# Kernel optimization log

Measured on AMD Instinct MI355X. Metric: run time of the kernel, lower is better.

Reference implementation:

```python
import math
import jax, jax.numpy as jnp
import numpy as np

N_ORDERS = 2
CHUNK = 64  # tokens per chunk (before virtual-token expansion)


def _expand_derivative(x, n):
    """expand_virtual_tokens(mode='derivative'): [B,H,S,D] -> [B,H,S*n,D]."""
    B, H, S, D = x.shape
    pad = jnp.zeros((B, H, n - 1, D), x.dtype)
    xp = jnp.concatenate([pad, x], axis=2)  # [B,H,S+n-1,D]
    coeffs = np.array([(-1) ** kk * math.comb(n - 1, kk) for kk in range(n)], dtype=np.float32)
    coeffs = coeffs / np.abs(coeffs).sum()  # L1-normalized binomial coeffs
    # window j at token t is x_pad[t+j]*coeffs[j]; then flip window dim (as in torch .flip(-1))
    win = jnp.stack([xp[:, :, j:j + S, :] * coeffs[j] for j in range(n)], axis=3)  # [B,H,S,n,D]
    win = win[:, :, :, ::-1, :]
    return win.reshape(B, H, S * n, D)


def _unlinear(x, scale=2.0):
    """unlinear_activation: gated norm-scaled gelu applied to inter-chunk state."""
    xn = jnp.linalg.norm(x, axis=-1, keepdims=True) + 1e-6
    return x / scale * jax.nn.gelu(scale * x / xn, approximate=True)


def _stab(x):
    # ensure_stability: clamp to [-1e4, 1e4], nan -> center (0)
    return jnp.nan_to_num(jnp.clip(x, -1e4, 1e4), nan=0.0, posinf=1e4, neginf=-1e4)


def _forward(q, k, v, beta):
    n = N_ORDERS
    B, H, S, D = q.shape
    qe = _expand_derivative(q, n)
    ke = _expand_derivative(k, n)
    ve = _expand_derivative(v, n)
    be = jnp.repeat(beta, n, axis=-1)[..., None]  # [B,H,S*n,1]
    w = ke * be  # delta-rule write keys
    u = ve * be  # delta-rule write values

    Cn = CHUNK * n                     # virtual tokens per chunk
    NC = (S * n) // Cn                 # number of chunks
    ch = lambda x: x.reshape(B, H, NC, Cn, D)
    qc, kc, wc, uc = ch(qe), ch(ke), ch(w), ch(u)

    # triangular (forward-substitution) inversion per chunk:
    # T = (I + tril(W K^T, -1))^{-1}  == fast_invert_matrix of the strictly-lower system
    A = jnp.tril(jnp.einsum('bhnid,bhnjd->bhnij', wc, kc), -1)
    eye = jnp.eye(Cn, dtype=q.dtype)
    T = jax.scipy.linalg.solve_triangular(
        eye + A, jnp.broadcast_to(eye, A.shape), lower=True, unit_diagonal=True)
    wci = jnp.einsum('bhnij,bhnjd->bhnid', T, wc)
    uci = jnp.einsum('bhnij,bhnjd->bhnid', T, uc)

    def chunk_step(h, xs):
        # sequential_delta_product_scan body: per-token Householder updates, n_orders steps
        qx, wx, ux = xs  # each [B,H,Cn,D]
        C = CHUNK
        qr = qx.reshape(B, H, C, n, D)
        wr = wx.reshape(B, H, C, n, D)
        ur = ux.reshape(B, H, C, n, D)
        state = jnp.broadcast_to(h[:, :, None], (B, H, C, D, D))  # per-token state
        outs = []
        for s in range(n):
            qs, ws, us = qr[:, :, :, s], wr[:, :, :, s], ur[:, :, :, s]
            kho = jnp.einsum('bhcd,bhcde->bhce', ws, state)
            uval = us - kho
            o_inter = jnp.einsum('bhcd,bhcde->bhce', qs, state)
            o_intra = qs * uval
            state = _stab(state + jnp.einsum('bhcd,bhce->bhcde', ws, uval))
            outs.append(o_intra + o_inter)
        o = jnp.stack(outs, axis=3).reshape(B, H, C * n, D)  # interleave: pos t*n+s
        h_new = _unlinear(state[:, :, -1])  # linear_activation=False path
        return h_new, o

    xs = (jnp.moveaxis(qc, 2, 0), jnp.moveaxis(wci, 2, 0), jnp.moveaxis(uci, 2, 0))
    h0 = jnp.zeros((B, H, D, D), q.dtype)
    _, os = jax.lax.scan(chunk_step, h0, xs)  # os: [NC,B,H,Cn,D]
    out_v = jnp.moveaxis(os, 0, 2).reshape(B, H, S, n, D)
    return out_v[..., n - 1, :]  # collapse virtual tokens: keep last-order output per token


def setup_inputs() -> dict:
    key = jax.random.key(0)
    kq, kk, kv, kb = jax.random.split(key, 4)
    B, H, S, D = 2, 16, 2048, 64
    return {
        'q': jax.random.normal(kq, (B, H, S, D), jnp.float32),
        'k': jax.random.normal(kk, (B, H, S, D), jnp.float32),
        'v': jax.random.normal(kv, (B, H, S, D), jnp.float32),
        'beta': jax.random.uniform(kb, (B, H, S), jnp.float32),
    }


def reference(q, k, v, beta):
    return _forward(q, k, v, beta)
```

## Files before the change

kernel.cpp:

```cpp
#include <hip/hip_runtime.h>
#include <math.h>


namespace {
constexpr int PAIRS = 32;
constexpr int SLEN  = 2048;
constexpr int D     = 64;
constexpr int CK    = 64;
constexpr int CN    = 128;
constexpr int NCH   = 32;
constexpr int NB2   = 16;
constexpr int NP    = 5;

__device__ __forceinline__ float stab1(float x) {
    float y = __builtin_amdgcn_fmed3f(x, -10000.f, 10000.f);
    return (x != x) ? 0.f : y;
}

__device__ __forceinline__ int kidx(int a, int f4) {
    return a * 68 + 4 * (f4 ^ ((a >> 2) & 3));
}
}

__global__ __launch_bounds__(512, 1)
void la_phase1(const float* __restrict__ kg, const float* __restrict__ vg,
               const float* __restrict__ bg, float* __restrict__ ws)
{
    __shared__ float Ysh[CN][CN];
    __shared__ float Gm[65][66];
    __shared__ char  ureg[36864];
    __shared__ float bq4[CK], bh[CK];

    float* kstf = (float*)ureg;
    float* scm  = (float*)ureg;
    float (*redsh)[3][8][CN] = (float(*)[3][8][CN])(ureg + 12288);

    const int blk  = blockIdx.x;
    const int p    = blk >> 5;
    const int nc   = blk & 31;
    const int tid  = threadIdx.x;
    const int baseT = nc * CK;
    const float* kp = kg + (size_t)p * SLEN * D;
    const float* vp = vg + (size_t)p * SLEN * D;
    const float* bp = bg + (size_t)p * SLEN;

    for (int u = tid; u < 65 * 16; u += 512) {
        int a = u >> 4, f4 = u & 15;
        int src = baseT - 1 + a;
        float4 val = float4{0.f, 0.f, 0.f, 0.f};
        if (src >= 0) val = ((const float4*)(kp + (size_t)src * D))[f4];
        *(float4*)&kstf[kidx(a, f4)] = val;
    }
    if (tid < CK) {
        float bv = bp[baseT + tid];
        bq4[tid] = 0.25f * bv;
        bh[tid]  = 0.5f  * bv;
    }
    __syncthreads();

    for (int u = tid; u < CN * 32; u += 512) {
        int i = u >> 5, f4i = u & 31;
        int ci = i >> 1, si = i & 1;
        float sc = si ? bh[ci] : -bh[ci];
        float4 val = float4{0.f, 0.f, 0.f, 0.f};
        if (f4i < 16) {
            val = *(const float4*)&kstf[kidx(ci - si + 1, f4i)];
        } else {
            int srcT = baseT + ci - si;
            if (srcT >= 0) val = ((const float4*)(vp + (size_t)srcT * D))[f4i - 16];
        }
        val.x *= sc; val.y *= sc; val.z *= sc; val.w *= sc;
        *(float4*)&Ysh[i][f4i * 4] = val;
    }

    for (int tt = tid; tt < 17 * 17; tt += 512) {
        int ta = tt / 17, tb = tt % 17;
        if (tb > ta) continue;
        int a0 = ta * 4, b0 = tb * 4;
        float acc[4][4] = {};
        for (int d4 = 0; d4 < 16; ++d4) {
            float4 av[4], bv[4];
            #pragma unroll
            for (int r = 0; r < 4; ++r) {
                av[r] = *(const float4*)&kstf[kidx(min(a0 + r, 64), d4)];
                bv[r] = *(const float4*)&kstf[kidx(min(b0 + r, 64), d4)];
            }
            #pragma unroll
            for (int r = 0; r < 4; ++r)
                #pragma unroll
                for (int c = 0; c < 4; ++c)
                    acc[r][c] += av[r].x * bv[c].x + av[r].y * bv[c].y
                               + av[r].z * bv[c].z + av[r].w * bv[c].w;
        }
        #pragma unroll
        for (int r = 0; r < 4; ++r)
            #pragma unroll
            for (int c = 0; c < 4; ++c)
                if (a0 + r <= 64 && b0 + c <= 64) {
                    Gm[a0 + r][b0 + c] = acc[r][c];
                    Gm[b0 + c][a0 + r] = acc[r][c];
                }
    }
    __syncthreads();

    for (int e = tid; e < 192; e += 512) {
        int gp = (e < 64) ? 0 : 1;
        int ee = e - gp * 64;
        int j = ee >> 3, r = ee & 7;
        int i = 8 * gp + r;
        int ai = (i >> 1) - (i & 1) + 1;
        int aj = (j >> 1) - (j & 1) + 1;
        float sgn = ((i ^ j) & 1) ? -1.f : 1.f;
        scm[(gp * CN + j) * 8 + r] = sgn * bq4[i >> 1] * Gm[ai][aj];
    }
    __syncthreads();

    const int col = tid & 127;
    const int grp = tid >> 7;

    for (int g = 0; g < 16; ++g) {
        const int bufG  = g % 3;
        const int bufG1 = (g + 1) % 3;
        const int bufG2 = (g + 2) % 3;

        if (grp == 0) {
            float acc[8] = {};
            if (g > 0) {
                #pragma unroll
                for (int r = 0; r < 8; ++r)
                    acc[r] = redsh[g & 1][0][r][col] + redsh[g & 1][1][r][col]
                           + redsh[g & 1][2][r][col];
                #pragma unroll
                for (int jj = 0; jj < 8; ++jj) {
                    int j = 8 * g - 8 + jj;
                    float yv = Ysh[j][col];
                    const float4 a03 = *(const float4*)&scm[(bufG * CN + j) * 8];
                    const float4 a47 = *(const float4*)&scm[(bufG * CN + j) * 8 + 4];
                    acc[0] += a03.x * yv; acc[1] += a03.y * yv;
                    acc[2] += a03.z * yv; acc[3] += a03.w * yv;
                    acc[4] += a47.x * yv; acc[5] += a47.y * yv;
                    acc[6] += a47.z * yv; acc[7] += a47.w * yv;
                }
            }
            float yn[8];
            #pragma unroll
            for (int r = 0; r < 8; ++r) {
                float val = Ysh[8 * g + r][col] - acc[r];
                #pragma unroll
                for (int rp = 0; rp < 8; ++rp)
                    if (rp < r) val -= scm[(bufG * CN + 8 * g + rp) * 8 + r] * yn[rp];
                yn[r] = val;
                Ysh[8 * g + r][col] = val;
            }
        } else {
            if (g + 2 <= 15) {
                int gb = g + 2, jmax = 8 * gb + 8;
                for (int e = tid - 128; e < 8 * jmax; e += 384) {
                    int j = e >> 3, r = e & 7;
                    int i = 8 * gb + r;
                    int ai = (i >> 1) - (i & 1) + 1;
                    int aj = (j >> 1) - (j & 1) + 1;
                    float sgn = ((i ^ j) & 1) ? -1.f : 1.f;
                    scm[(bufG2 * CN + j) * 8 + r] = sgn * bq4[i >> 1] * Gm[ai][aj];
                }
            }
            if (g + 1 <= 15) {
                float acc[8] = {};
                for (int j = grp - 1; j < 8 * g; j += 3) {
                    float yv = Ysh[j][col];
                    const float4 a03 = *(const float4*)&scm[(bufG1 * CN + j) * 8];
                    const float4 a47 = *(const float4*)&scm[(bufG1 * CN + j) * 8 + 4];
                    acc[0] += a03.x * yv; acc[1] += a03.y * yv;
                    acc[2] += a03.z * yv; acc[3] += a03.w * yv;
                    acc[4] += a47.x * yv; acc[5] += a47.y * yv;
                    acc[6] += a47.z * yv; acc[7] += a47.w * yv;
                }
                #pragma unroll
                for (int r = 0; r < 8; ++r)
                    redsh[(g + 1) & 1][grp - 1][r][col] = acc[r];
            }
        }
        __syncthreads();
    }

    float* gY = ws + (size_t)(p * NCH + nc) * (CN * CN);
    for (int u = tid; u < CN * 32; u += 512) {
        int r = u >> 5, f4 = u & 31;
        *(float4*)&gY[r * CN + f4 * 4] = *(const float4*)&Ysh[r][f4 * 4];
    }
}

__global__ __launch_bounds__(512, 4)
void la_phase2(const float* __restrict__ qg, const float* __restrict__ ws,
               float* __restrict__ outg)
{
    __shared__ float WU[2][NP][256];
    __shared__ float Qs[2][NP][64];
    __shared__ float pR1[8][NP][64];
    __shared__ float pKH[8][NP][64];
    __shared__ float pOA[8][NP][64];
    __shared__ float UV0[NP][64];
    __shared__ float UV1r[64];
    __shared__ float hsh[64][67];

    const int blk  = blockIdx.x;
    const int p    = blk >> 4, nb = blk & 15;
    const int tid  = threadIdx.x;
    const int w    = tid >> 6, lane = tid & 63;
    const int hd   = tid >> 3;
    const int he0  = (tid & 7) * 8;

    const float* qp = qg + (size_t)p * SLEN * D;
    float* op = outg + (size_t)p * SLEN * D;
    const float* wsbase = ws + (size_t)p * NCH * (CN * CN);

    const int cMain = nb * 4 + w;

    float4 wuR = float4{0.f, 0.f, 0.f, 0.f};
    float  qR  = 0.f;

    auto stage_load = [&](int nc) {
        const float* gY = wsbase + (size_t)nc * (CN * CN);
        if (w < 4) {
            wuR = *(const float4*)(gY + (size_t)(2 * cMain) * CN + lane * 4);
            int t = nc * CK + cMain;
            qR = qp[(size_t)((t > 0) ? t - 1 : 0) * D + lane];
        } else if (w == 4) {
            wuR = *(const float4*)(gY + (size_t)126 * CN + lane * 4);
            qR = qp[(size_t)(nc * CK + 62) * D + lane];
        }
    };
    auto stage_write = [&](int buf) {
        if (w < NP) {
            *(float4*)&WU[buf][w][lane * 4] = wuR;
            Qs[buf][w][lane] = qR;
        }
    };

    for (int idx = tid; idx < 64 * 67; idx += 512) (&hsh[0][0])[idx] = 0.f;
    stage_load(0);
    stage_write(0);
    __syncthreads();

    for (int nc = 0; nc < NCH; ++nc) {
        const int buf = nc & 1;

        float hs[8];
        #pragma unroll
        for (int j = 0; j < 8; ++j) hs[j] = hsh[8 * w + j][lane];

        if (nc + 1 < NCH) stage_load(nc + 1);

        #pragma unroll
        for (int P = 0; P < NP; ++P) {
            float4 a = *(const float4*)&WU[buf][P][8 * w];
            float4 b = *(const float4*)&WU[buf][P][8 * w + 4];
            pR1[w][P][lane] =
                  ((a.x * hs[0] + a.y * hs[1]) + (a.z * hs[2] + a.w * hs[3]))
                + ((b.x * hs[4] + b.y * hs[5]) + (b.z * hs[6] + b.w * hs[7]));
        }
        __syncthreads();

        if (w < NP) {
            float s = 0.f;
            #pragma unroll
            for (int wv = 0; wv < 8; ++wv) s += pR1[wv][w][lane];
            UV0[w][lane] = WU[buf][w][64 + lane] - s;
        }
        __syncthreads();

        #pragma unroll
        for (int P = 0; P < NP; ++P) {
            float uv0 = UV0[P][lane];
            float4 w0a = *(const float4*)&WU[buf][P][8 * w];
            float4 w0b = *(const float4*)&WU[buf][P][8 * w + 4];
            float4 w1a = *(const float4*)&WU[buf][P][128 + 8 * w];
            float4 w1b = *(const float4*)&WU[buf][P][128 + 8 * w + 4];
            float4 qa  = *(const float4*)&Qs[buf][P][8 * w];
            float4 qb  = *(const float4*)&Qs[buf][P][8 * w + 4];
            float st0 = stab1(hs[0] + w0a.x * uv0);
            float st1 = stab1(hs[1] + w0a.y * uv0);
            float st2 = stab1(hs[2] + w0a.z * uv0);
            float st3 = stab1(hs[3] + w0a.w * uv0);
            float st4 = stab1(hs[4] + w0b.x * uv0);
            float st5 = stab1(hs[5] + w0b.y * uv0);
            float st6 = stab1(hs[6] + w0b.z * uv0);
            float st7 = stab1(hs[7] + w0b.w * uv0);
            pKH[w][P][lane] =
                  ((w1a.x * st0 + w1a.y * st1) + (w1a.z * st2 + w1a.w * st3))
                + ((w1b.x * st4 + w1b.y * st5) + (w1b.z * st6 + w1b.w * st7));
            pOA[w][P][lane] =
                  ((qa.x * st0 + qa.y * st1) + (qa.z * st2 + qa.w * st3))
                + ((qb.x * st4 + qb.y * st5) + (qb.z * st6 + qb.w * st7));
        }
        stage_write(buf ^ 1);
        __syncthreads();

        if (w < 4) {
            float skh = 0.f, soa = 0.f;
            #pragma unroll
            for (int wv = 0; wv < 8; ++wv) {
                skh += pKH[wv][w][lane];
                soa += pOA[wv][w][lane];
            }
            float uv1 = WU[buf][w][192 + lane] - skh;
            int t = nc * CK + cMain;
            float outv = 0.5f * (Qs[buf][w][lane] * uv1 + soa);
            op[(size_t)t * D + lane] = (t > 0) ? outv : 0.f;
        } else if (w == 4) {
            float skh = 0.f;
            #pragma unroll
            for (int wv = 0; wv < 8; ++wv) skh += pKH[wv][4][lane];
            UV1r[lane] = WU[buf][4][192 + lane] - skh;
        }
        __syncthreads();

        {
            float w0d = WU[buf][4][hd];
            float w1d = WU[buf][4][128 + hd];
            float st2v[8];
            float ssum = 0.f;
            #pragma unroll
            for (int j = 0; j < 8; ++j) {
                float st1 = stab1(hsh[hd][he0 + j] + w0d * UV0[4][he0 + j]);
                float st2 = stab1(st1 + w1d * UV1r[he0 + j]);
                st2v[j] = st2;
                ssum += st2 * st2;
            }
            ssum += __shfl_xor(ssum, 1);
            ssum += __shfl_xor(ssum, 2);
            ssum += __shfl_xor(ssum, 4);
            float xn = __builtin_amdgcn_sqrtf(ssum) + 1e-6f;
            float s2 = 2.f * __builtin_amdgcn_rcpf(xn);
            #pragma unroll
            for (int j = 0; j < 8; ++j) {
                float x  = st2v[j];
                float y  = x * s2;
                float y2 = y * y;
                float e  = __builtin_amdgcn_exp2f(y * (2.3022078f + 0.1029432f * y2));
                float th = (e - 1.f) * __builtin_amdgcn_rcpf(e + 1.f);
                hsh[hd][he0 + j] = 0.25f * x * y * (1.f + th);
            }
        }
        __syncthreads();
    }
}

extern "C" void kernel_launch(void* const* d_in, const int* in_sizes, int n_in,
                              void* d_out, int out_size, void* d_ws, size_t ws_size,
                              hipStream_t stream)
{
    (void)in_sizes; (void)n_in; (void)out_size; (void)ws_size;
    const float* q    = (const float*)d_in[0];
    const float* k    = (const float*)d_in[1];
    const float* v    = (const float*)d_in[2];
    const float* beta = (const float*)d_in[3];
    float* ws  = (float*)d_ws;
    float* out = (float*)d_out;

    la_phase1<<<PAIRS * NCH, 512, 0, stream>>>(k, v, beta, ws);
    la_phase2<<<PAIRS * NB2, 512, 0, stream>>>(q, ws, out);
}
```

Baseline: 275.1 us.

## Split phase-1 triangular solve across two blocks by column half

Result: no change. 280.5 us (+2.0%).

```diff
diff --git a/kernel.cpp b/kernel.cpp
--- a/kernel.cpp
+++ b/kernel.cpp
@@ -22,29 +22,30 @@
 }
 }
 
-__global__ __launch_bounds__(512, 1)
+__global__ __launch_bounds__(256, 2)
 void la_phase1(const float* __restrict__ kg, const float* __restrict__ vg,
                const float* __restrict__ bg, float* __restrict__ ws)
 {
-    __shared__ float Ysh[CN][CN];
+    __shared__ float Ysh[CN][68];
     __shared__ float Gm[65][66];
-    __shared__ char  ureg[36864];
+    __shared__ char  ureg[24576];
     __shared__ float bq4[CK], bh[CK];
 
     float* kstf = (float*)ureg;
     float* scm  = (float*)ureg;
-    float (*redsh)[3][8][CN] = (float(*)[3][8][CN])(ureg + 12288);
+    float (*redsh)[3][8][64] = (float(*)[3][8][64])(ureg + 12288);
 
     const int blk  = blockIdx.x;
-    const int p    = blk >> 5;
-    const int nc   = blk & 31;
+    const int p    = blk >> 6;
+    const int nc   = (blk >> 1) & 31;
+    const int half = blk & 1;
     const int tid  = threadIdx.x;
     const int baseT = nc * CK;
     const float* kp = kg + (size_t)p * SLEN * D;
     const float* vp = vg + (size_t)p * SLEN * D;
     const float* bp = bg + (size_t)p * SLEN;
 
-    for (int u = tid; u < 65 * 16; u += 512) {
+    for (int u = tid; u < 65 * 16; u += 256) {
         int a = u >> 4, f4 = u & 15;
         int src = baseT - 1 + a;
         float4 val = float4{0.f, 0.f, 0.f, 0.f};
@@ -58,22 +59,22 @@
     }
     __syncthreads();
 
-    for (int u = tid; u < CN * 32; u += 512) {
-        int i = u >> 5, f4i = u & 31;
+    for (int u = tid; u < CN * 16; u += 256) {
+        int i = u >> 4, f4 = u & 15;
         int ci = i >> 1, si = i & 1;
         float sc = si ? bh[ci] : -bh[ci];
         float4 val = float4{0.f, 0.f, 0.f, 0.f};
-        if (f4i < 16) {
-            val = *(const float4*)&kstf[kidx(ci - si + 1, f4i)];
+        if (half == 0) {
+            val = *(const float4*)&kstf[kidx(ci - si + 1, f4)];
         } else {
             int srcT = baseT + ci - si;
-            if (srcT >= 0) val = ((const float4*)(vp + (size_t)srcT * D))[f4i - 16];
+            if (srcT >= 0) val = ((const float4*)(vp + (size_t)srcT * D))[f4];
         }
         val.x *= sc; val.y *= sc; val.z *= sc; val.w *= sc;
-        *(float4*)&Ysh[i][f4i * 4] = val;
-    }
-
-    for (int tt = tid; tt < 17 * 17; tt += 512) {
+        *(float4*)&Ysh[i][f4 * 4] = val;
+    }
+
+    for (int tt = tid; tt < 17 * 17; tt += 256) {
         int ta = tt / 17, tb = tt % 17;
         if (tb > ta) continue;
         int a0 = ta * 4, b0 = tb * 4;
@@ -103,7 +104,7 @@
     }
     __syncthreads();
 
-    for (int e = tid; e < 192; e += 512) {
+    for (int e = tid; e < 192; e += 256) {
         int gp = (e < 64) ? 0 : 1;
         int ee = e - gp * 64;
         int j = ee >> 3, r = ee & 7;
@@ -115,15 +116,15 @@
     }
     __syncthreads();
 
-    const int col = tid & 127;
-    const int grp = tid >> 7;
+    const int col = tid & 63;
+    const int m   = tid >> 6;
 
     for (int g = 0; g < 16; ++g) {
         const int bufG  = g % 3;
         const int bufG1 = (g + 1) % 3;
         const int bufG2 = (g + 2) % 3;
 
-        if (grp == 0) {
+        if (m == 0) {
             float acc[8] = {};
             if (g > 0) {
                 #pragma unroll
@@ -155,7 +156,7 @@
         } else {
             if (g + 2 <= 15) {
                 int gb = g + 2, jmax = 8 * gb + 8;
-                for (int e = tid - 128; e < 8 * jmax; e += 384) {
+                for (int e = tid - 64; e < 8 * jmax; e += 192) {
                     int j = e >> 3, r = e & 7;
                     int i = 8 * gb + r;
                     int ai = (i >> 1) - (i & 1) + 1;
@@ -166,7 +167,32 @@
             }
             if (g + 1 <= 15) {
                 float acc[8] = {};
-                for (int j = grp - 1; j < 8 * g; j += 3) {
+                const int len = (8 * g + 2) / 3;
+                const int lo = (m - 1) * len;
+                const int hi = min(8 * g, lo + len);
+                int j = lo;
+                for (; j + 4 <= hi; j += 4) {
+                    float y0 = Ysh[j][col], y1 = Ysh[j + 1][col];
+                    float y2 = Ysh[j + 2][col], y3 = Ysh[j + 3][col];
+                    const float* s0 = &scm[(bufG1 * CN + j) * 8];
+                    const float4 a0 = *(const float4*)(s0);
+                    const float4 b0 = *(const float4*)(s0 + 4);
+                    const float4 a1 = *(const float4*)(s0 + 8);
+                    const float4 b1 = *(const float4*)(s0 + 12);
+                    const float4 a2 = *(const float4*)(s0 + 16);
+                    const float4 b2 = *(const float4*)(s0 + 20);
+                    const float4 a3 = *(const float4*)(s0 + 24);
+                    const float4 b3 = *(const float4*)(s0 + 28);
+                    acc[0] += a0.x * y0 + a1.x * y1 + a2.x * y2 + a3.x * y3;
+                    acc[1] += a0.y * y0 + a1.y * y1 + a2.y * y2 + a3.y * y3;
+                    acc[2] += a0.z * y0 + a1.z * y1 + a2.z * y2 + a3.z * y3;
+                    acc[3] += a0.w * y0 + a1.w * y1 + a2.w * y2 + a3.w * y3;
+                    acc[4] += b0.x * y0 + b1.x * y1 + b2.x * y2 + b3.x * y3;
+                    acc[5] += b0.y * y0 + b1.y * y1 + b2.y * y2 + b3.y * y3;
+                    acc[6] += b0.z * y0 + b1.z * y1 + b2.z * y2 + b3.z * y3;
+                    acc[7] += b0.w * y0 + b1.w * y1 + b2.w * y2 + b3.w * y3;
+                }
+                for (; j < hi; ++j) {
                     float yv = Ysh[j][col];
                     const float4 a03 = *(const float4*)&scm[(bufG1 * CN + j) * 8];
                     const float4 a47 = *(const float4*)&scm[(bufG1 * CN + j) * 8 + 4];
@@ -177,15 +203,15 @@
                 }
                 #pragma unroll
                 for (int r = 0; r < 8; ++r)
-                    redsh[(g + 1) & 1][grp - 1][r][col] = acc[r];
-            }
-        }
-        __syncthreads();
-    }
-
-    float* gY = ws + (size_t)(p * NCH + nc) * (CN * CN);
-    for (int u = tid; u < CN * 32; u += 512) {
-        int r = u >> 5, f4 = u & 31;
+                    redsh[(g + 1) & 1][m - 1][r][col] = acc[r];
+            }
+        }
+        __syncthreads();
+    }
+
+    float* gY = ws + (size_t)(p * NCH + nc) * (CN * CN) + half * 64;
+    for (int u = tid; u < CN * 16; u += 256) {
+        int r = u >> 4, f4 = u & 15;
         *(float4*)&gY[r * CN + f4 * 4] = *(const float4*)&Ysh[r][f4 * 4];
     }
 }
@@ -358,6 +384,6 @@
     float* ws  = (float*)d_ws;
     float* out = (float*)d_out;
 
-    la_phase1<<<PAIRS * NCH, 512, 0, stream>>>(k, v, beta, ws);
+    la_phase1<<<PAIRS * NCH * 2, 256, 0, stream>>>(k, v, beta, ws);
     la_phase2<<<PAIRS * NB2, 512, 0, stream>>>(q, ws, out);
 }
```

## Keep phase-1 triangular-solve rows in registers and shrink block to 256 threads

Applied to the files above, without the earlier changes.

New measurement: 439.2 us. 1.6x slower.

```diff
diff --git a/kernel.cpp b/kernel.cpp
--- a/kernel.cpp
+++ b/kernel.cpp
@@ -20,31 +20,54 @@
 __device__ __forceinline__ int kidx(int a, int f4) {
     return a * 68 + 4 * (f4 ^ ((a >> 2) & 3));
 }
-}
-
-__global__ __launch_bounds__(512, 1)
+
+template<int GI>
+__device__ __forceinline__ void solve_group(float (&y0)[32], float (&y1)[32],
+                                            float (&accA)[8], float (&accB)[8],
+                                            const float* scmDiag) {
+    float yn0[8], yn1[8];
+    #pragma unroll
+    for (int r = 0; r < 8; ++r) {
+        float v0 = y0[GI * 8 + r] - accA[r];
+        float v1 = y1[GI * 8 + r] - accB[r];
+        #pragma unroll
+        for (int rp = 0; rp < 8; ++rp) {
+            if (rp < r) {
+                float a = scmDiag[rp * 8 + r];
+                v0 -= a * yn0[rp];
+                v1 -= a * yn1[rp];
+            }
+        }
+        yn0[r] = v0; yn1[r] = v1;
+        y0[GI * 8 + r] = v0; y1[GI * 8 + r] = v1;
+    }
+}
+}
+
+__global__ __launch_bounds__(256, 3)
 void la_phase1(const float* __restrict__ kg, const float* __restrict__ vg,
                const float* __restrict__ bg, float* __restrict__ ws)
 {
-    __shared__ float Ysh[CN][CN];
     __shared__ float Gm[65][66];
-    __shared__ char  ureg[36864];
+    __shared__ char  uni[28672];
     __shared__ float bq4[CK], bh[CK];
 
-    float* kstf = (float*)ureg;
-    float* scm  = (float*)ureg;
-    float (*redsh)[3][8][CN] = (float(*)[3][8][CN])(ureg + 12288);
+    float* kstf = (float*)uni;
+    float* scm  = (float*)uni;
+    float (*redsh)[8][CN] = (float(*)[8][CN])(uni + 12288);
 
     const int blk  = blockIdx.x;
     const int p    = blk >> 5;
     const int nc   = blk & 31;
     const int tid  = threadIdx.x;
+    const int lane = tid & 63;
+    const int m    = tid >> 6;
     const int baseT = nc * CK;
     const float* kp = kg + (size_t)p * SLEN * D;
     const float* vp = vg + (size_t)p * SLEN * D;
     const float* bp = bg + (size_t)p * SLEN;
 
-    for (int u = tid; u < 65 * 16; u += 512) {
+    for (int u = tid; u < 65 * 16; u += 256) {
         int a = u >> 4, f4 = u & 15;
         int src = baseT - 1 + a;
         float4 val = float4{0.f, 0.f, 0.f, 0.f};
@@ -58,22 +81,7 @@
     }
     __syncthreads();
 
-    for (int u = tid; u < CN * 32; u += 512) {
-        int i = u >> 5, f4i = u & 31;
-        int ci = i >> 1, si = i & 1;
-        float sc = si ? bh[ci] : -bh[ci];
-        float4 val = float4{0.f, 0.f, 0.f, 0.f};
-        if (f4i < 16) {
-            val = *(const float4*)&kstf[kidx(ci - si + 1, f4i)];
-        } else {
-            int srcT = baseT + ci - si;
-            if (srcT >= 0) val = ((const float4*)(vp + (size_t)srcT * D))[f4i - 16];
-        }
-        val.x *= sc; val.y *= sc; val.z *= sc; val.w *= sc;
-        *(float4*)&Ysh[i][f4i * 4] = val;
-    }
-
-    for (int tt = tid; tt < 17 * 17; tt += 512) {
+    for (int tt = tid; tt < 17 * 17; tt += 256) {
         int ta = tt / 17, tb = tt % 17;
         if (tb > ta) continue;
         int a0 = ta * 4, b0 = tb * 4;
@@ -101,9 +109,34 @@
                     Gm[b0 + c][a0 + r] = acc[r][c];
                 }
     }
+
+    float y0[32], y1[32];
+    #pragma unroll
+    for (int gi = 0; gi < 4; ++gi) {
+        #pragma unroll
+        for (int r8 = 0; r8 < 8; ++r8) {
+            int i = 8 * (4 * gi + m) + r8;
+            int ci = i >> 1, si = i & 1;
+            float sc = si ? bh[ci] : -bh[ci];
+            float2 val;
+            if (lane < 32) {
+                int a = ci - si + 1;
+                int e = 2 * lane;
+                int idx = a * 68 + 4 * ((e >> 2) ^ ((a >> 2) & 3)) + (e & 3);
+                val = *(const float2*)&kstf[idx];
+            } else {
+                int srcT = baseT + ci - si;
+                int e = 2 * (lane - 32);
+                if (srcT >= 0) val = *(const float2*)&vp[(size_t)srcT * D + e];
+                else           val = float2{0.f, 0.f};
+            }
+            y0[gi * 8 + r8] = sc * val.x;
+            y1[gi * 8 + r8] = sc * val.y;
+        }
+    }
     __syncthreads();
 
-    for (int e = tid; e < 192; e += 512) {
+    for (int e = tid; e < 192; e += 256) {
         int gp = (e < 64) ? 0 : 1;
         int ee = e - gp * 64;
         int j = ee >> 3, r = ee & 7;
@@ -115,79 +148,80 @@
     }
     __syncthreads();
 
-    const int col = tid & 127;
-    const int grp = tid >> 7;
-
     for (int g = 0; g < 16; ++g) {
-        const int bufG  = g % 3;
-        const int bufG1 = (g + 1) % 3;
-        const int bufG2 = (g + 2) % 3;
-
-        if (grp == 0) {
-            float acc[8] = {};
+        const int s = g & 3;
+        if (m == s) {
+            float accA[8] = {}, accB[8] = {};
             if (g > 0) {
                 #pragma unroll
-                for (int r = 0; r < 8; ++r)
-                    acc[r] = redsh[g & 1][0][r][col] + redsh[g & 1][1][r][col]
-                           + redsh[g & 1][2][r][col];
-                #pragma unroll
-                for (int jj = 0; jj < 8; ++jj) {
-                    int j = 8 * g - 8 + jj;
-                    float yv = Ysh[j][col];
-                    const float4 a03 = *(const float4*)&scm[(bufG * CN + j) * 8];
-                    const float4 a47 = *(const float4*)&scm[(bufG * CN + j) * 8 + 4];
-                    acc[0] += a03.x * yv; acc[1] += a03.y * yv;
-                    acc[2] += a03.z * yv; acc[3] += a03.w * yv;
-                    acc[4] += a47.x * yv; acc[5] += a47.y * yv;
-                    acc[6] += a47.z * yv; acc[7] += a47.w * yv;
+                for (int wv = 0; wv < 4; ++wv)
+                    #pragma unroll
+                    for (int r = 0; r < 8; ++r) {
+                        float2 t = *(const float2*)&redsh[wv][r][2 * lane];
+                        accA[r] += t.x; accB[r] += t.y;
+                    }
+            }
+            const float* scmDiag = scm + (((g % 3) * CN + 8 * g) * 8);
+            const int gq = g >> 2;
+            if      (gq == 0) solve_group<0>(y0, y1, accA, accB, scmDiag);
+            else if (gq == 1) solve_group<1>(y0, y1, accA, accB, scmDiag);
+            else if (gq == 2) solve_group<2>(y0, y1, accA, accB, scmDiag);
+            else              solve_group<3>(y0, y1, accA, accB, scmDiag);
+        } else if (g + 2 <= 15) {
+            const int T2 = g + 2, bufB = T2 % 3;
+            const int br = (m < s ? m : m - 1) * 64 + lane;
+            const int nel = 8 * (8 * T2 + 8);
+            for (int e = br; e < nel; e += 192) {
+                int j = e >> 3, r = e & 7;
+                int i = 8 * T2 + r;
+                int ai = (i >> 1) - (i & 1) + 1;
+                int aj = (j >> 1) - (j & 1) + 1;
+                float sgn = ((i ^ j) & 1) ? -1.f : 1.f;
+                scm[(bufB * CN + j) * 8 + r] = sgn * bq4[i >> 1] * Gm[ai][aj];
+            }
+        }
+        __syncthreads();
+
+        if (g < 15) {
+            const int bufT = (g + 1) % 3;
+            float accA[8] = {}, accB[8] = {};
+            #pragma unroll
+            for (int gi = 0; gi < 4; ++gi) {
+                if (4 * gi + m <= g) {
+                    #pragma unroll
+                    for (int r8 = 0; r8 < 8; ++r8) {
+                        int j = 8 * (4 * gi + m) + r8;
+                        const float* sp = &scm[(bufT * CN + j) * 8];
+                        const float4 a03 = *(const float4*)(sp);
+                        const float4 a47 = *(const float4*)(sp + 4);
+                        float yv0 = y0[gi * 8 + r8], yv1 = y1[gi * 8 + r8];
+                        accA[0] += a03.x * yv0; accB[0] += a03.x * yv1;
+                        accA[1] += a03.y * yv0; accB[1] += a03.y * yv1;
+                        accA[2] += a03.z * yv0; accB[2] += a03.z * yv1;
+                        accA[3] += a03.w * yv0; accB[3] += a03.w * yv1;
+                        accA[4] += a47.x * yv0; accB[4] += a47.x * yv1;
+                        accA[5] += a47.y * yv0; accB[5] += a47.y * yv1;
+                        accA[6] += a47.z * yv0; accB[6] += a47.z * yv1;
+                        accA[7] += a47.w * yv0; accB[7] += a47.w * yv1;
+                    }
                 }
             }
-            float yn[8];
-            #pragma unroll
-            for (int r = 0; r < 8; ++r) {
-                float val = Ysh[8 * g + r][col] - acc[r];
-                #pragma unroll
-                for (int rp = 0; rp < 8; ++rp)
-                    if (rp < r) val -= scm[(bufG * CN + 8 * g + rp) * 8 + r] * yn[rp];
-                yn[r] = val;
-                Ysh[8 * g + r][col] = val;
-            }
-        } else {
-            if (g + 2 <= 15) {
-                int gb = g + 2, jmax = 8 * gb + 8;
-                for (int e = tid - 128; e < 8 * jmax; e += 384) {
-                    int j = e >> 3, r = e & 7;
-                    int i = 8 * gb + r;
-                    int ai = (i >> 1) - (i & 1) + 1;
-                    int aj = (j >> 1) - (j & 1) + 1;
-                    float sgn = ((i ^ j) & 1) ? -1.f : 1.f;
-                    scm[(bufG2 * CN + j) * 8 + r] = sgn * bq4[i >> 1] * Gm[ai][aj];
-                }
-            }
-            if (g + 1 <= 15) {
-                float acc[8] = {};
-                for (int j = grp - 1; j < 8 * g; j += 3) {
-                    float yv = Ysh[j][col];
-                    const float4 a03 = *(const float4*)&scm[(bufG1 * CN + j) * 8];
-                    const float4 a47 = *(const float4*)&scm[(bufG1 * CN + j) * 8 + 4];
-                    acc[0] += a03.x * yv; acc[1] += a03.y * yv;
-                    acc[2] += a03.z * yv; acc[3] += a03.w * yv;
-                    acc[4] += a47.x * yv; acc[5] += a47.y * yv;
-                    acc[6] += a47.z * yv; acc[7] += a47.w * yv;
-                }
-                #pragma unroll
-                for (int r = 0; r < 8; ++r)
-                    redsh[(g + 1) & 1][grp - 1][r][col] = acc[r];
-            }
+            #pragma unroll
+            for (int r = 0; r < 8; ++r)
+                *(float2*)&redsh[m][r][2 * lane] = float2{accA[r], accB[r]};
         }
         __syncthreads();
     }
 
     float* gY = ws + (size_t)(p * NCH + nc) * (CN * CN);
-    for (int u = tid; u < CN * 32; u += 512) {
-        int r = u >> 5, f4 = u & 31;
-        *(float4*)&gY[r * CN + f4 * 4] = *(const float4*)&Ysh[r][f4 * 4];
-    }
+    #pragma unroll
+    for (int gi = 0; gi < 4; ++gi)
+        #pragma unroll
+        for (int r8 = 0; r8 < 8; ++r8) {
+            int j = 8 * (4 * gi + m) + r8;
+            *(float2*)&gY[(size_t)j * CN + 2 * lane] =
+                float2{y0[gi * 8 + r8], y1[gi * 8 + r8]};
+        }
 }
 
 __global__ __launch_bounds__(512, 4)
@@ -358,6 +392,6 @@
     float* ws  = (float*)d_ws;
     float* out = (float*)d_out;
 
-    la_phase1<<<PAIRS * NCH, 512, 0, stream>>>(k, v, beta, ws);
+    la_phase1<<<PAIRS * NCH, 256, 0, stream>>>(k, v, beta, ws);
     la_phase2<<<PAIRS * NB2, 512, 0, stream>>>(q, ws, out);
 }
```

## Split phase-1 triangular solve across two blocks per chunk by column half

Applied to the files above, without the earlier changes.

New measurement: 347.3 us. +26.3%, slower.

```diff
diff --git a/kernel.cpp b/kernel.cpp
--- a/kernel.cpp
+++ b/kernel.cpp
@@ -22,23 +22,26 @@
 }
 }
 
-__global__ __launch_bounds__(512, 1)
+__global__ __launch_bounds__(512, 2)
 void la_phase1(const float* __restrict__ kg, const float* __restrict__ vg,
                const float* __restrict__ bg, float* __restrict__ ws)
 {
-    __shared__ float Ysh[CN][CN];
-    __shared__ float Gm[65][66];
-    __shared__ char  ureg[36864];
+    __shared__ float Ysh[CN][65];
+    __shared__ float Gm[65][72];
+    __shared__ char  uni[26624];
     __shared__ float bq4[CK], bh[CK];
 
-    float* kstf = (float*)ureg;
-    float* scm  = (float*)ureg;
-    float (*redsh)[3][8][CN] = (float(*)[3][8][CN])(ureg + 12288);
+    float* kstf = (float*)uni;
+    float* scm  = (float*)uni;
+    float (*redsh)[64][9] = (float(*)[64][9])(uni + 8192);
 
     const int blk  = blockIdx.x;
-    const int p    = blk >> 5;
-    const int nc   = blk & 31;
+    const int p    = blk >> 6;
+    const int nc   = (blk >> 1) & 31;
+    const int half = blk & 1;
     const int tid  = threadIdx.x;
+    const int lane = tid & 63;
+    const int m    = tid >> 6;
     const int baseT = nc * CK;
     const float* kp = kg + (size_t)p * SLEN * D;
     const float* vp = vg + (size_t)p * SLEN * D;
@@ -58,19 +61,19 @@
     }
     __syncthreads();
 
-    for (int u = tid; u < CN * 32; u += 512) {
-        int i = u >> 5, f4i = u & 31;
+    for (int u = tid; u < CN * 16; u += 512) {
+        int i = u >> 4, f4 = u & 15;
         int ci = i >> 1, si = i & 1;
         float sc = si ? bh[ci] : -bh[ci];
         float4 val = float4{0.f, 0.f, 0.f, 0.f};
-        if (f4i < 16) {
-            val = *(const float4*)&kstf[kidx(ci - si + 1, f4i)];
+        if (half == 0) {
+            val = *(const float4*)&kstf[kidx(ci - si + 1, f4)];
         } else {
             int srcT = baseT + ci - si;
-            if (srcT >= 0) val = ((const float4*)(vp + (size_t)srcT * D))[f4i - 16];
+            if (srcT >= 0) val = ((const float4*)(vp + (size_t)srcT * D))[f4];
         }
         val.x *= sc; val.y *= sc; val.z *= sc; val.w *= sc;
-        *(float4*)&Ysh[i][f4i * 4] = val;
+        *(float4*)&Ysh[i][f4 * 4] = val;
     }
 
     for (int tt = tid; tt < 17 * 17; tt += 512) {
@@ -103,89 +106,80 @@
     }
     __syncthreads();
 
-    for (int e = tid; e < 192; e += 512) {
-        int gp = (e < 64) ? 0 : 1;
-        int ee = e - gp * 64;
-        int j = ee >> 3, r = ee & 7;
-        int i = 8 * gp + r;
+    for (int e = tid; e < 64; e += 512) {
+        int j = e >> 3, r = e & 7;
+        int i = r;
         int ai = (i >> 1) - (i & 1) + 1;
         int aj = (j >> 1) - (j & 1) + 1;
         float sgn = ((i ^ j) & 1) ? -1.f : 1.f;
-        scm[(gp * CN + j) * 8 + r] = sgn * bq4[i >> 1] * Gm[ai][aj];
+        scm[j * 8 + r] = sgn * bq4[i >> 1] * Gm[ai][aj];
     }
     __syncthreads();
 
-    const int col = tid & 127;
-    const int grp = tid >> 7;
-
     for (int g = 0; g < 16; ++g) {
-        const int bufG  = g % 3;
-        const int bufG1 = (g + 1) % 3;
-        const int bufG2 = (g + 2) % 3;
-
-        if (grp == 0) {
+        const int s = g & 7;
+        if (m == s) {
             float acc[8] = {};
             if (g > 0) {
                 #pragma unroll
-                for (int r = 0; r < 8; ++r)
-                    acc[r] = redsh[g & 1][0][r][col] + redsh[g & 1][1][r][col]
-                           + redsh[g & 1][2][r][col];
-                #pragma unroll
-                for (int jj = 0; jj < 8; ++jj) {
-                    int j = 8 * g - 8 + jj;
-                    float yv = Ysh[j][col];
-                    const float4 a03 = *(const float4*)&scm[(bufG * CN + j) * 8];
-                    const float4 a47 = *(const float4*)&scm[(bufG * CN + j) * 8 + 4];
-                    acc[0] += a03.x * yv; acc[1] += a03.y * yv;
-                    acc[2] += a03.z * yv; acc[3] += a03.w * yv;
-                    acc[4] += a47.x * yv; acc[5] += a47.y * yv;
-                    acc[6] += a47.z * yv; acc[7] += a47.w * yv;
+                for (int wv = 0; wv < 8; ++wv) {
+                    float4 t0 = *(const float4*)&redsh[wv][lane][0];
+                    float4 t1 = *(const float4*)&redsh[wv][lane][4];
+                    acc[0] += t0.x; acc[1] += t0.y; acc[2] += t0.z; acc[3] += t0.w;
+                    acc[4] += t1.x; acc[5] += t1.y; acc[6] += t1.z; acc[7] += t1.w;
                 }
             }
+            const float* sd = &scm[(((g & 1) * CN) + 8 * g) * 8];
             float yn[8];
             #pragma unroll
             for (int r = 0; r < 8; ++r) {
-                float val = Ysh[8 * g + r][col] - acc[r];
+                float val = Ysh[8 * g + r][lane] - acc[r];
                 #pragma unroll
                 for (int rp = 0; rp < 8; ++rp)
-                    if (rp < r) val -= scm[(bufG * CN + 8 * g + rp) * 8 + r] * yn[rp];
+                    if (rp < r) val -= sd[rp * 8 + r] * yn[rp];
                 yn[r] = val;
-                Ysh[8 * g + r][col] = val;
-            }
-        } else {
-            if (g + 2 <= 15) {
-                int gb = g + 2, jmax = 8 * gb + 8;
-                for (int e = tid - 128; e < 8 * jmax; e += 384) {
-                    int j = e >> 3, r = e & 7;
-                    int i = 8 * gb + r;
-                    int ai = (i >> 1) - (i & 1) + 1;
-                    int aj = (j >> 1) - (j & 1) + 1;
-                    float sgn = ((i ^ j) & 1) ? -1.f : 1.f;
-                    scm[(bufG2 * CN + j) * 8 + r] = sgn * bq4[i >> 1] * Gm[ai][aj];
-                }
-            }
-            if (g + 1 <= 15) {
-                float acc[8] = {};
-                for (int j = grp - 1; j < 8 * g; j += 3) {
-                    float yv = Ysh[j][col];
-                    const float4 a03 = *(const float4*)&scm[(bufG1 * CN + j) * 8];
-                    const float4 a47 = *(const float4*)&scm[(bufG1 * CN + j) * 8 + 4];
-                    acc[0] += a03.x * yv; acc[1] += a03.y * yv;
-                    acc[2] += a03.z * yv; acc[3] += a03.w * yv;
-                    acc[4] += a47.x * yv; acc[5] += a47.y * yv;
-                    acc[6] += a47.z * yv; acc[7] += a47.w * yv;
-                }
-                #pragma unroll
-                for (int r = 0; r < 8; ++r)
-                    redsh[(g + 1) & 1][grp - 1][r][col] = acc[r];
-            }
-        }
-        __syncthreads();
-    }
-
-    float* gY = ws + (size_t)(p * NCH + nc) * (CN * CN);
-    for (int u = tid; u < CN * 32; u += 512) {
-        int r = u >> 5, f4 = u & 31;
+                Ysh[8 * g + r][lane] = val;
+            }
+        } else if (g + 1 <= 15) {
+            const int T = g + 1, bufB = T & 1;
+            const int nel = 8 * (8 * T + 8);
+            const int br = (m < s ? m : m - 1) * 64 + lane;
+            for (int e = br; e < nel; e += 448) {
+                int j = e >> 3, r = e & 7;
+                int i = 8 * T + r;
+                int ai = (i >> 1) - (i & 1) + 1;
+                int aj = (j >> 1) - (j & 1) + 1;
+                float sgn = ((i ^ j) & 1) ? -1.f : 1.f;
+                scm[(bufB * CN + j) * 8 + r] = sgn * bq4[i >> 1] * Gm[ai][aj];
+            }
+        }
+        __syncthreads();
+
+        if (g < 15) {
+            const int bufT = (g + 1) & 1;
+            const int len = g + 1;
+            const int lo = m * len;
+            const int hi = lo + len;
+            float acc[8] = {};
+            for (int j = lo; j < hi; ++j) {
+                float yv = Ysh[j][lane];
+                const float* sp = &scm[(bufT * CN + j) * 8];
+                const float4 a03 = *(const float4*)(sp);
+                const float4 a47 = *(const float4*)(sp + 4);
+                acc[0] += a03.x * yv; acc[1] += a03.y * yv;
+                acc[2] += a03.z * yv; acc[3] += a03.w * yv;
+                acc[4] += a47.x * yv; acc[5] += a47.y * yv;
+                acc[6] += a47.z * yv; acc[7] += a47.w * yv;
+            }
+            *(float4*)&redsh[m][lane][0] = float4{acc[0], acc[1], acc[2], acc[3]};
+            *(float4*)&redsh[m][lane][4] = float4{acc[4], acc[5], acc[6], acc[7]};
+        }
+        __syncthreads();
+    }
+
+    float* gY = ws + (size_t)(p * NCH + nc) * (CN * CN) + half * 64;
+    for (int u = tid; u < CN * 16; u += 512) {
+        int r = u >> 4, f4 = u & 15;
         *(float4*)&gY[r * CN + f4 * 4] = *(const float4*)&Ysh[r][f4 * 4];
     }
 }
@@ -194,14 +188,13 @@
 void la_phase2(const float* __restrict__ qg, const float* __restrict__ ws,
                float* __restrict__ outg)
 {
-    __shared__ float WU[2][NP][256];
-    __shared__ float Qs[2][NP][64];
-    __shared__ float pR1[8][NP][64];
-    __shared__ float pKH[8][NP][64];
-    __shared__ float pOA[8][NP][64];
-    __shared__ float UV0[NP][64];
-    __shared__ float UV1r[64];
-    __shared__ float hsh[64][67];
+    __shared__ float  WU[2][NP][256];
+    __shared__ float  Qs[2][NP][64];
+    __shared__ float  pR1[8][NP][64];
+    __shared__ float2 pKO[8][NP][64];
+    __shared__ float  UV0[NP][64];
+    __shared__ float  UV1r[64];
+    __shared__ float  hsh[64][67];
 
     const int blk  = blockIdx.x;
     const int p    = blk >> 4, nb = blk & 15;
@@ -251,10 +244,12 @@
 
         if (nc + 1 < NCH) stage_load(nc + 1);
 
+        float4 w0aR[NP], w0bR[NP];
         #pragma unroll
         for (int P = 0; P < NP; ++P) {
             float4 a = *(const float4*)&WU[buf][P][8 * w];
             float4 b = *(const float4*)&WU[buf][P][8 * w + 4];
+            w0aR[P] = a; w0bR[P] = b;
             pR1[w][P][lane] =
                   ((a.x * hs[0] + a.y * hs[1]) + (a.z * hs[2] + a.w * hs[3]))
                 + ((b.x * hs[4] + b.y * hs[5]) + (b.z * hs[6] + b.w * hs[7]));
@@ -272,8 +267,8 @@
         #pragma unroll
         for (int P = 0; P < NP; ++P) {
             float uv0 = UV0[P][lane];
-            float4 w0a = *(const float4*)&WU[buf][P][8 * w];
-            float4 w0b = *(const float4*)&WU[buf][P][8 * w + 4];
+            float4 w0a = w0aR[P];
+            float4 w0b = w0bR[P];
             float4 w1a = *(const float4*)&WU[buf][P][128 + 8 * w];
             float4 w1b = *(const float4*)&WU[buf][P][128 + 8 * w + 4];
             float4 qa  = *(const float4*)&Qs[buf][P][8 * w];
@@ -286,12 +281,11 @@
             float st5 = stab1(hs[5] + w0b.y * uv0);
             float st6 = stab1(hs[6] + w0b.z * uv0);
             float st7 = stab1(hs[7] + w0b.w * uv0);
-            pKH[w][P][lane] =
-                  ((w1a.x * st0 + w1a.y * st1) + (w1a.z * st2 + w1a.w * st3))
-                + ((w1b.x * st4 + w1b.y * st5) + (w1b.z * st6 + w1b.w * st7));
-            pOA[w][P][lane] =
-                  ((qa.x * st0 + qa.y * st1) + (qa.z * st2 + qa.w * st3))
-                + ((qb.x * st4 + qb.y * st5) + (qb.z * st6 + qb.w * st7));
+            float kh = ((w1a.x * st0 + w1a.y * st1) + (w1a.z * st2 + w1a.w * st3))
+                     + ((w1b.x * st4 + w1b.y * st5) + (w1b.z * st6 + w1b.w * st7));
+            float oa = ((qa.x * st0 + qa.y * st1) + (qa.z * st2 + qa.w * st3))
+                     + ((qb.x * st4 + qb.y * st5) + (qb.z * st6 + qb.w * st7));
+            pKO[w][P][lane] = float2{kh, oa};
         }
         stage_write(buf ^ 1);
         __syncthreads();
@@ -300,8 +294,8 @@
             float skh = 0.f, soa = 0.f;
             #pragma unroll
             for (int wv = 0; wv < 8; ++wv) {
-                skh += pKH[wv][w][lane];
-                soa += pOA[wv][w][lane];
+                float2 t = pKO[wv][w][lane];
+                skh += t.x; soa += t.y;
             }
             float uv1 = WU[buf][w][192 + lane] - skh;
             int t = nc * CK + cMain;
@@ -310,7 +304,7 @@
         } else if (w == 4) {
             float skh = 0.f;
             #pragma unroll
-            for (int wv = 0; wv < 8; ++wv) skh += pKH[wv][4][lane];
+            for (int wv = 0; wv < 8; ++wv) skh += pKO[wv][4][lane].x;
             UV1r[lane] = WU[buf][4][192 + lane] - skh;
         }
         __syncthreads();
@@ -358,6 +352,6 @@
     float* ws  = (float*)d_ws;
     float* out = (float*)d_out;
 
-    la_phase1<<<PAIRS * NCH, 512, 0, stream>>>(k, v, beta, ws);
+    la_phase1<<<PAIRS * NCH * 2, 512, 0, stream>>>(k, v, beta, ws);
     la_phase2<<<PAIRS * NB2, 512, 0, stream>>>(q, ws, out);
 }
```
